# Kernel tuning notes

Hardware: AMD Instinct MI355X
Metric: run time of the kernel (lower is better)

The kernel has to match this reference:

```python
import jax, jax.numpy as jnp
import numpy as np


def _gelu(v):
    return jax.nn.gelu(v, approximate=False)


def _conv1x1(x, W, b):
    # x: [B, Ci, H, W], W: [Co, Ci]
    return jnp.einsum('bixy,oi->boxy', x, W) + b[None, :, None, None]


def _spectral(x, w1r, w2r, m1, m2):
    # x: [B, Ci, H, W]; w*r: [Ci, Co, m1, m2, 2] (real/imag)
    w1 = w1r[..., 0] + 1j * w1r[..., 1]
    w2 = w2r[..., 0] + 1j * w2r[..., 1]
    B, C, H, W = x.shape
    xf = jnp.fft.rfft2(x)  # [B, Ci, H, W//2+1] complex64
    o1 = jnp.einsum('bixy,ioxy->boxy', xf[:, :, :m1, :m2], w1)
    o2 = jnp.einsum('bixy,ioxy->boxy', xf[:, :, H - m1:, :m2], w2)
    Co = w1.shape[1]
    of = jnp.zeros((B, Co, H, W // 2 + 1), dtype=xf.dtype)
    of = of.at[:, :, :m1, :m2].set(o1)
    of = of.at[:, :, H - m1:, :m2].set(o2)
    return jnp.fft.irfft2(of, s=(H, W))


def _pool(x):
    B, C, H, W = x.shape
    return x.reshape(B, C, H // 2, 2, W // 2, 2).mean(axis=(3, 5))


def _up(x):
    # matches torch F.interpolate(scale_factor=2, mode='bilinear', align_corners=False)
    B, C, H, W = x.shape
    return jax.image.resize(x, (B, C, 2 * H, 2 * W), method='bilinear')


def _forward(x, fcin_w, fcin_b, sc1_w1, sc1_w2, c1_w, c1_b, sc2_w1, sc2_w2, c2_w, c2_b,
             scb_w1, scb_w2, cb_w, cb_b, su2_w1, su2_w2, u2_w, u2_b,
             su1_w1, su1_w2, u1_w, u1_b, fc1_w, fc1_b, fc2_w, fc2_b):
    v = jnp.einsum('bhwi,oi->bhwo', x, fcin_w) + fcin_b   # lift 6 -> width
    v = v.transpose(0, 3, 1, 2)                            # [B, C, H, W]
    x1 = _gelu(_spectral(v, sc1_w1, sc1_w2, 12, 12) + _conv1x1(v, c1_w, c1_b))
    x1d = _pool(x1)
    x2 = _gelu(_spectral(x1d, sc2_w1, sc2_w2, 8, 8) + _conv1x1(x1d, c2_w, c2_b))
    x2d = _pool(x2)
    xb = _gelu(_spectral(x2d, scb_w1, scb_w2, 4, 4) + _conv1x1(x2d, cb_w, cb_b))
    x2c = jnp.concatenate([_up(xb), x2], axis=1)           # [B, 3.5w, H/2, W/2]
    x2o = _gelu(_spectral(x2c, su2_w1, su2_w2, 8, 8) + _conv1x1(x2c, u2_w, u2_b))
    x1c = jnp.concatenate([_up(x2o), x1], axis=1)          # [B, 2.5w, H, W]
    x1o = _gelu(_spectral(x1c, su1_w1, su1_w2, 12, 12) + _conv1x1(x1c, u1_w, u1_b))
    h = x1o.transpose(0, 2, 3, 1)
    h = _gelu(jnp.einsum('bhwi,oi->bhwo', h, fc1_w) + fc1_b)
    return jnp.einsum('bhwi,oi->bhwo', h, fc2_w) + fc2_b   # [B, H, W, 3]


def setup_inputs() -> dict:
    key = jax.random.key(0)
    ks = jax.random.split(key, 20)

    def cw(k, ci, co, m):  # complex spectral weight stored as [...,2] real
        return (1.0 / (ci * co)) * jax.random.normal(k, (ci, co, m, m, 2), dtype=jnp.float32)

    def lin(k, o, i):
        k1, k2 = jax.random.split(k)
        lim = 1.0 / np.sqrt(i)
        return (jax.random.uniform(k1, (o, i), jnp.float32, -lim, lim),
                jax.random.uniform(k2, (o,), jnp.float32, -lim, lim))

    d = {}
    d['x'] = jax.random.normal(ks[0], (4, 256, 256, 6), dtype=jnp.float32)
    d['fcin_w'], d['fcin_b'] = lin(ks[1], 64, 6)
    d['sc1_w1'] = cw(ks[2], 64, 64, 12); d['sc1_w2'] = cw(ks[3], 64, 64, 12)
    d['c1_w'], d['c1_b'] = lin(ks[4], 64, 64)
    d['sc2_w1'] = cw(ks[5], 64, 96, 8); d['sc2_w2'] = cw(ks[6], 64, 96, 8)
    d['c2_w'], d['c2_b'] = lin(ks[7], 96, 64)
    d['scb_w1'] = cw(ks[8], 96, 128, 4); d['scb_w2'] = cw(ks[9], 96, 128, 4)
    d['cb_w'], d['cb_b'] = lin(ks[10], 128, 96)
    d['su2_w1'] = cw(ks[11], 224, 96, 8); d['su2_w2'] = cw(ks[12], 224, 96, 8)
    d['u2_w'], d['u2_b'] = lin(ks[13], 96, 224)
    d['su1_w1'] = cw(ks[14], 160, 64, 12); d['su1_w2'] = cw(ks[15], 160, 64, 12)
    d['u1_w'], d['u1_b'] = lin(ks[16], 64, 160)
    d['fc1_w'], d['fc1_b'] = lin(ks[17], 256, 64)
    d['fc2_w'], d['fc2_b'] = lin(ks[18], 3, 256)
    return d


def reference(x, fcin_w, fcin_b, sc1_w1, sc1_w2, c1_w, c1_b, sc2_w1, sc2_w2, c2_w, c2_b,
              scb_w1, scb_w2, cb_w, cb_b, su2_w1, su2_w2, u2_w, u2_b,
              su1_w1, su1_w2, u1_w, u1_b, fc1_w, fc1_b, fc2_w, fc2_b):
    return _forward(x, fcin_w, fcin_b, sc1_w1, sc1_w2, c1_w, c1_b, sc2_w1, sc2_w2, c2_w, c2_b,
                    scb_w1, scb_w2, cb_w, cb_b, su2_w1, su2_w2, u2_w, u2_b,
                    su1_w1, su1_w2, u1_w, u1_b, fc1_w, fc1_b, fc2_w, fc2_b)
```

## Files before the change

### kernel.cpp

```cpp
#include <hip/hip_runtime.h>
#include <math.h>
#include <cstdio>


__device__ __forceinline__ float gelu_f(float v) {
    return 0.5f * v * (1.0f + erff(v * 0.70710678118654752f));
}

__global__ __launch_bounds__(256) void init_tw_kernel(float2* tw) {
    int t = threadIdx.x;
    tw[t] = make_float2(cospif(t * (1.0f / 128.0f)), sinpif(t * (1.0f / 128.0f)));
}

__global__ __launch_bounds__(256) void transpose_mat_kernel(const float* __restrict__ src,
                                                            float* __restrict__ dst,
                                                            int Co, int Ci) {
    int idx = blockIdx.x * blockDim.x + threadIdx.x;
    if (idx >= Ci * Co) return;
    int o = idx % Co; int i = idx / Co;
    dst[idx] = src[(size_t)o * Ci + i];
}

template <int M2, int SRC>
__global__ __launch_bounds__(64, 4) void dftx_kernel(
    const float* __restrict__ U, int C, int Coff, int Ctot,
    int H, int W, int Hs, int Ws,
    const float* __restrict__ liftW, const float* __restrict__ liftB,
    int stepW, const float2* __restrict__ tw, float2* __restrict__ Fx) {
    __shared__ float twc[256], tws[256];
    for (int t = threadIdx.x; t < 256; t += blockDim.x) {
        float2 v = tw[t]; twc[t] = v.x; tws[t] = v.y;
    }
    __syncthreads();
    int by = blockIdx.x;
    int c = blockIdx.y * 64 + threadIdx.x;
    if (c >= C) return;

    const float* rowD = nullptr;
    const float* Sa = nullptr; const float* Sb = nullptr;
    float wy = 0.f, bc = 0.f;
    float w6[6] = {0, 0, 0, 0, 0, 0};
    if constexpr (SRC == 0) {
        rowD = U + (size_t)by * W * C + c;
    } else if constexpr (SRC == 1) {
        bc = liftB[c];
#pragma unroll
        for (int j = 0; j < 6; j++) w6[j] = liftW[c * 6 + j];
    } else {
        int b = by / H, y = by % H;
        float fy = 0.5f * y - 0.25f;
        int y0 = (int)floorf(fy); wy = fy - y0;
        int ya = y0 < 0 ? 0 : y0;
        int yb = (y0 + 1 > Hs - 1) ? Hs - 1 : y0 + 1;
        Sa = U + ((size_t)(b * Hs + ya) * Ws) * C + c;
        Sb = U + ((size_t)(b * Hs + yb) * Ws) * C + c;
    }

    float ar[M2], ai[M2];
#pragma unroll
    for (int k = 0; k < M2; k++) { ar[k] = 0.f; ai[k] = 0.f; }
    for (int x = 0; x < W; x++) {
        float u;
        if constexpr (SRC == 0) {
            u = rowD[(size_t)x * C];
        } else if constexpr (SRC == 1) {
            const float* xp = U + ((size_t)by * W + x) * 6;
            u = bc;
#pragma unroll
            for (int j = 0; j < 6; j++) u += w6[j] * xp[j];
        } else {
            float fx = 0.5f * x - 0.25f;
            int x0 = (int)floorf(fx); float wx = fx - x0;
            int xa = x0 < 0 ? 0 : x0;
            int xb2 = (x0 + 1 > Ws - 1) ? Ws - 1 : x0 + 1;
            float va = Sa[(size_t)xa * C] * (1.f - wx) + Sa[(size_t)xb2 * C] * wx;
            float vb = Sb[(size_t)xa * C] * (1.f - wx) + Sb[(size_t)xb2 * C] * wx;
            u = va * (1.f - wy) + vb * wy;
        }
        int tb = (x * stepW) & 255;
        int t = 0;
#pragma unroll
        for (int k = 0; k < M2; k++) {
            ar[k] += u * twc[t];
            ai[k] -= u * tws[t];
            t = (t + tb) & 255;
        }
    }
    float2* o = Fx + ((size_t)by * M2) * Ctot + Coff + c;
#pragma unroll
    for (int k = 0; k < M2; k++) o[(size_t)k * Ctot] = make_float2(ar[k], ai[k]);
}

__global__ __launch_bounds__(256, 4) void dfty_kernel(
    const float2* __restrict__ Fx, int H, int m1, int m2, int Ct,
    int stepH, const float2* __restrict__ tw, float2* __restrict__ XF, int N) {
    __shared__ float twc[256], tws[256];
    for (int t = threadIdx.x; t < 256; t += blockDim.x) {
        float2 v = tw[t]; twc[t] = v.x; tws[t] = v.y;
    }
    __syncthreads();
    int idx = blockIdx.x * blockDim.x + threadIdx.x;
    if (idx >= N) return;
    int c = idx % Ct; int r = idx / Ct;
    int kx = r % m2;  r /= m2;
    int kyi = r % (2 * m1); int b = r / (2 * m1);
    int ky = (kyi < m1) ? kyi : (H - 2 * m1 + kyi);
    int tstep = (ky * stepH) & 255;
    const float2* base = Fx + ((size_t)(b * H) * m2 + kx) * Ct + c;
    size_t stride = (size_t)m2 * Ct;
    float accr = 0.f, acci = 0.f;
    int t = 0;
    for (int y = 0; y < H; y++) {
        float2 f = base[(size_t)y * stride];
        float cc = twc[t], ss = tws[t];
        accr += f.x * cc + f.y * ss;
        acci += f.y * cc - f.x * ss;
        t = (t + tstep) & 255;
    }
    XF[idx] = make_float2(accr, acci);
}

__global__ __launch_bounds__(128, 2) void modemix2_kernel(
    const float2* __restrict__ XF,
    const float* __restrict__ w1f, const float* __restrict__ w2f,
    int Ci, int Co, int m1, int m2, float2* __restrict__ OF) {
    __shared__ float2 xsm[4][224];
    int mode = blockIdx.x;
    int nmode = 2 * m1 * m2;
    for (int t = threadIdx.x; t < 4 * Ci; t += blockDim.x) {
        int b = t / Ci, i = t - b * Ci;
        xsm[b][i] = XF[((size_t)b * nmode + mode) * Ci + i];
    }
    __syncthreads();
    int o = threadIdx.x;
    if (o >= Co) return;
    int kx = mode % m2; int kyi = mode / m2;
    const float2* w = (const float2*)((kyi < m1) ? w1f : w2f);
    int ky = (kyi < m1) ? kyi : (kyi - m1);
    float ar0 = 0, ai0 = 0, ar1 = 0, ai1 = 0, ar2 = 0, ai2 = 0, ar3 = 0, ai3 = 0;
    for (int i = 0; i < Ci; i++) {
        float2 wv = w[(((size_t)i * Co + o) * m1 + ky) * m2 + kx];
        float2 a = xsm[0][i], b2 = xsm[1][i], c2 = xsm[2][i], d2 = xsm[3][i];
        ar0 += a.x * wv.x - a.y * wv.y;  ai0 += a.x * wv.y + a.y * wv.x;
        ar1 += b2.x * wv.x - b2.y * wv.y; ai1 += b2.x * wv.y + b2.y * wv.x;
        ar2 += c2.x * wv.x - c2.y * wv.y; ai2 += c2.x * wv.y + c2.y * wv.x;
        ar3 += d2.x * wv.x - d2.y * wv.y; ai3 += d2.x * wv.y + d2.y * wv.x;
    }
    OF[((size_t)0 * nmode + mode) * Co + o] = make_float2(ar0, ai0);
    OF[((size_t)1 * nmode + mode) * Co + o] = make_float2(ar1, ai1);
    OF[((size_t)2 * nmode + mode) * Co + o] = make_float2(ar2, ai2);
    OF[((size_t)3 * nmode + mode) * Co + o] = make_float2(ar3, ai3);
}

__global__ __launch_bounds__(256, 4) void idfty_kernel(
    const float2* __restrict__ OF, int H, int m1, int m2, int Co,
    int stepH, const float2* __restrict__ tw, float2* __restrict__ Gy, int N) {
    __shared__ float twc[256], tws[256];
    for (int t = threadIdx.x; t < 256; t += blockDim.x) {
        float2 v = tw[t]; twc[t] = v.x; tws[t] = v.y;
    }
    __syncthreads();
    int idx = blockIdx.x * blockDim.x + threadIdx.x;
    if (idx >= N) return;
    int o = idx % Co; int r = idx / Co;
    int kx = r % m2;  r /= m2;
    int y = r % H;    int b = r / H;
    float accr = 0.f, acci = 0.f;
    for (int kyi = 0; kyi < 2 * m1; kyi++) {
        int ky = (kyi < m1) ? kyi : (H - 2 * m1 + kyi);
        int t = (ky * y * stepH) & 255;
        float2 f = OF[((size_t)(b * 2 * m1 + kyi) * m2 + kx) * Co + o];
        float cc = twc[t], ss = tws[t];
        accr += f.x * cc - f.y * ss;
        acci += f.x * ss + f.y * cc;
    }
    Gy[idx] = make_float2(accr, acci);
}

template <int SRCA, bool HASB, bool HEAD, int CO, int G, int PPG, int CIMAX>
__global__ __launch_bounds__(CO * G, 2) void synth_kernel(
    const float2* __restrict__ Gy,
    const float* __restrict__ A, int CA, int HsA, int WsA,
    const float* __restrict__ UB, int CB,
    const float* __restrict__ liftW, const float* __restrict__ liftB,
    const float* __restrict__ WcT, const float* __restrict__ bias,
    int H, int W, int m2, int stepW, float invHW,
    const float2* __restrict__ tw, float* __restrict__ out,
    const float* __restrict__ fc1t, const float* __restrict__ fc1b,
    const float* __restrict__ fc2w, const float* __restrict__ fc2b) {
    constexpr int P = G * PPG;
    constexpr int BLK = CO * G;
    __shared__ float twc[256], tws[256];
    __shared__ float xs[P][CIMAX];
    __shared__ float hid[HEAD ? P * 256 : 1];
    int tid = threadIdx.x;
    for (int t = tid; t < 256; t += BLK) {
        float2 v = tw[t]; twc[t] = v.x; tws[t] = v.y;
    }
    const int Ci = CA + (HASB ? CB : 0);
    int pix0 = blockIdx.x * P;
    for (int t = tid; t < P * Ci; t += BLK) {
        int p = t / Ci, i = t - p * Ci;
        int pix = pix0 + p;
        float val;
        if (HASB && i >= CA) {
            val = UB[(size_t)pix * CB + (i - CA)];
        } else if constexpr (SRCA == 0) {
            val = A[(size_t)pix * CA + i];
        } else if constexpr (SRCA == 1) {
            const float* xp = A + (size_t)pix * 6;
            float a = liftB[i];
#pragma unroll
            for (int j = 0; j < 6; j++) a += xp[j] * liftW[i * 6 + j];
            val = a;
        } else {
            int x = pix % W; int r = pix / W; int y = r % H; int b = r / H;
            float fy = 0.5f * y - 0.25f, fx = 0.5f * x - 0.25f;
            int y0 = (int)floorf(fy); float wy = fy - y0;
            int x0 = (int)floorf(fx); float wx = fx - x0;
            int ya = y0 < 0 ? 0 : y0;
            int yb = (y0 + 1 > HsA - 1) ? HsA - 1 : y0 + 1;
            int xa = x0 < 0 ? 0 : x0;
            int xb2 = (x0 + 1 > WsA - 1) ? WsA - 1 : x0 + 1;
            const float* base = A + ((size_t)b * HsA * WsA) * CA + i;
            float v00 = base[((size_t)ya * WsA + xa) * CA];
            float v01 = base[((size_t)ya * WsA + xb2) * CA];
            float v10 = base[((size_t)yb * WsA + xa) * CA];
            float v11 = base[((size_t)yb * WsA + xb2) * CA];
            val = (1.f - wy) * ((1.f - wx) * v00 + wx * v01) +
                  wy * ((1.f - wx) * v10 + wx * v11);
        }
        xs[p][i] = val;
    }
    __syncthreads();
    int o = tid % CO, g = tid / CO;
    int x0 = pix0 % W;  int by = pix0 / W;
    int xg = x0 + g * PPG;
    float acc[PPG];
#pragma unroll
    for (int q = 0; q < PPG; q++) acc[q] = 0.f;
    const float2* grow = Gy + ((size_t)by * m2) * CO + o;
    int base = (xg * stepW) & 255;
    for (int k = 0; k < m2; k++) {
        float2 gv = grow[(size_t)k * CO];
        float sc = (k == 0) ? 1.f : 2.f;
        float gx = sc * gv.x, gyv = sc * gv.y;
        int dk = (k * stepW) & 255;
        int t = (base * k) & 255;
#pragma unroll
        for (int q = 0; q < PPG; q++) {
            acc[q] += gx * twc[t] - gyv * tws[t];
            t = (t + dk) & 255;
        }
    }
#pragma unroll
    for (int q = 0; q < PPG; q++) acc[q] *= invHW;
    for (int i = 0; i < Ci; i++) {
        float w = WcT[(size_t)i * CO + o];
#pragma unroll
        for (int q = 0; q < PPG; q++) acc[q] += xs[g * PPG + q][i] * w;
    }
    float bb = bias[o];
    if constexpr (!HEAD) {
#pragma unroll
        for (int q = 0; q < PPG; q++) {
            int pix = pix0 + g * PPG + q;
            out[(size_t)pix * CO + o] = gelu_f(acc[q] + bb);
        }
    } else {
        float gout[PPG];
#pragma unroll
        for (int q = 0; q < PPG; q++) gout[q] = gelu_f(acc[q] + bb);
        __syncthreads();
        float* act = &xs[0][0];
#pragma unroll
        for (int q = 0; q < PPG; q++) act[(g * PPG + q) * 64 + o] = gout[q];
        __syncthreads();
        int j = tid;
        float h[P];
        float c1 = fc1b[j];
#pragma unroll
        for (int p = 0; p < P; p++) h[p] = c1;
        for (int i = 0; i < 64; i++) {
            float w = fc1t[i * 256 + j];
#pragma unroll
            for (int p = 0; p < P; p++) h[p] += act[p * 64 + i] * w;
        }
#pragma unroll
        for (int p = 0; p < P; p++) hid[p * 256 + j] = gelu_f(h[p]);
        __syncthreads();
        if (tid < P * 12) {
            int sub = tid & 3; int d = tid >> 2;
            int o3 = d % 3, p = d / 3;
            const float* hr = hid + p * 256;
            const float* wr = fc2w + o3 * 256;
            float a = 0.f;
            for (int i = sub; i < 256; i += 4) a += hr[i] * wr[i];
            a += __shfl_xor(a, 1);
            a += __shfl_xor(a, 2);
            if (sub == 0) out[(size_t)(pix0 + p) * 3 + o3] = a + fc2b[o3];
        }
    }
}

__global__ __launch_bounds__(256, 4) void pool_kernel(
    const float* __restrict__ in, float* __restrict__ out,
    int H2, int W2, int C, int N) {
    int idx = blockIdx.x * blockDim.x + threadIdx.x;
    if (idx >= N) return;
    int c = idx % C; int r = idx / C;
    int xo = r % W2; r /= W2;
    int yo = r % H2; int b = r / H2;
    int W = W2 * 2;
    const float* p = in + (((size_t)(b * (H2 * 2) + 2 * yo) * W) + 2 * xo) * C + c;
    float v = p[0] + p[C] + p[(size_t)W * C] + p[(size_t)W * C + C];
    out[idx] = 0.25f * v;
}


static inline unsigned nb_(size_t n, int b) { return (unsigned)((n + b - 1) / b); }

extern "C" void kernel_launch(void* const* d_in, const int* in_sizes, int n_in,
                              void* d_out, int out_size, void* d_ws, size_t ws_size,
                              hipStream_t stream) {
    (void)in_sizes; (void)n_in; (void)out_size;
    const float* x      = (const float*)d_in[0];
    const float* fcin_w = (const float*)d_in[1];
    const float* fcin_b = (const float*)d_in[2];
    const float* sc1_w1 = (const float*)d_in[3];
    const float* sc1_w2 = (const float*)d_in[4];
    const float* c1_w   = (const float*)d_in[5];
    const float* c1_b   = (const float*)d_in[6];
    const float* sc2_w1 = (const float*)d_in[7];
    const float* sc2_w2 = (const float*)d_in[8];
    const float* c2_w   = (const float*)d_in[9];
    const float* c2_b   = (const float*)d_in[10];
    const float* scb_w1 = (const float*)d_in[11];
    const float* scb_w2 = (const float*)d_in[12];
    const float* cb_w   = (const float*)d_in[13];
    const float* cb_b   = (const float*)d_in[14];
    const float* su2_w1 = (const float*)d_in[15];
    const float* su2_w2 = (const float*)d_in[16];
    const float* u2_w   = (const float*)d_in[17];
    const float* u2_b   = (const float*)d_in[18];
    const float* su1_w1 = (const float*)d_in[19];
    const float* su1_w2 = (const float*)d_in[20];
    const float* u1_w   = (const float*)d_in[21];
    const float* u1_b   = (const float*)d_in[22];
    const float* fc1_w  = (const float*)d_in[23];
    const float* fc1_b  = (const float*)d_in[24];
    const float* fc2_w  = (const float*)d_in[25];
    const float* fc2_b  = (const float*)d_in[26];
    float* out = (float*)d_out;

    float* wsf = (float*)d_ws;
    size_t off = 0;
    auto alloc = [&](size_t nfloats) -> float* {
        float* p = wsf + off;
        off += (nfloats + 63) & ~(size_t)63;
        return p;
    };

    float2* tw = (float2*)alloc(512);
    float* c1t  = alloc(64 * 64);
    float* c2t  = alloc(64 * 96);
    float* cbt  = alloc(96 * 128);
    float* u2t  = alloc(224 * 96);
    float* u1t  = alloc(160 * 64);
    float* fc1t = alloc(64 * 256);

    float* x1  = alloc((size_t)4 * 256 * 256 * 64);
    float* x1d = alloc((size_t)4 * 128 * 128 * 64);
    float* x2  = alloc((size_t)4 * 128 * 128 * 96);
    float* xb  = alloc((size_t)4 * 64 * 64 * 128);
    float* x2o = alloc((size_t)4 * 128 * 128 * 96);

    float2* Fx = (float2*)alloc((size_t)2 * 4 * 256 * 12 * 160);
    float2* XF = (float2*)alloc((size_t)2 * 4 * 24 * 12 * 160);
    float2* OF = (float2*)alloc((size_t)2 * 4 * 24 * 12 * 128);
    float2* Gy = (float2*)alloc((size_t)2 * 4 * 256 * 12 * 96);

    size_t need = off * sizeof(float);
    if (ws_size < need) {
        fprintf(stderr, "[FNO2d] workspace too small: need %zu bytes, have %zu\n",
                need, ws_size);
        return;
    }
    float* x2d = x1d;

    init_tw_kernel<<<1, 256, 0, stream>>>(tw);
    transpose_mat_kernel<<<nb_(64 * 64, 256), 256, 0, stream>>>(c1_w, c1t, 64, 64);
    transpose_mat_kernel<<<nb_(64 * 96, 256), 256, 0, stream>>>(c2_w, c2t, 96, 64);
    transpose_mat_kernel<<<nb_(96 * 128, 256), 256, 0, stream>>>(cb_w, cbt, 128, 96);
    transpose_mat_kernel<<<nb_(224 * 96, 256), 256, 0, stream>>>(u2_w, u2t, 96, 224);
    transpose_mat_kernel<<<nb_(160 * 64, 256), 256, 0, stream>>>(u1_w, u1t, 64, 160);
    transpose_mat_kernel<<<nb_(64 * 256, 256), 256, 0, stream>>>(fc1_w, fc1t, 256, 64);

    int N;

    dftx_kernel<12, 1><<<dim3(1024, 1), 64, 0, stream>>>(
        x, 64, 0, 64, 256, 256, 0, 0, fcin_w, fcin_b, 1, tw, Fx);
    N = 4 * 24 * 12 * 64;
    dfty_kernel<<<nb_(N, 256), 256, 0, stream>>>(Fx, 256, 12, 12, 64, 1, tw, XF, N);
    modemix2_kernel<<<288, 128, 0, stream>>>(XF, sc1_w1, sc1_w2, 64, 64, 12, 12, OF);
    N = 4 * 256 * 12 * 64;
    idfty_kernel<<<nb_(N, 256), 256, 0, stream>>>(OF, 256, 12, 12, 64, 1, tw, Gy, N);
    synth_kernel<1, false, false, 64, 4, 4, 64><<<4 * 256 * 256 / 16, 256, 0, stream>>>(
        Gy, x, 64, 0, 0, nullptr, 0, fcin_w, fcin_b, c1t, c1_b,
        256, 256, 12, 1, 1.0f / 65536.0f, tw, x1,
        nullptr, nullptr, nullptr, nullptr);
    N = 4 * 128 * 128 * 64;
    pool_kernel<<<nb_(N, 256), 256, 0, stream>>>(x1, x1d, 128, 128, 64, N);

    dftx_kernel<8, 0><<<dim3(512, 1), 64, 0, stream>>>(
        x1d, 64, 0, 64, 128, 128, 0, 0, nullptr, nullptr, 2, tw, Fx);
    N = 4 * 16 * 8 * 64;
    dfty_kernel<<<nb_(N, 256), 256, 0, stream>>>(Fx, 128, 8, 8, 64, 2, tw, XF, N);
    modemix2_kernel<<<128, 128, 0, stream>>>(XF, sc2_w1, sc2_w2, 64, 96, 8, 8, OF);
    N = 4 * 128 * 8 * 96;
    idfty_kernel<<<nb_(N, 256), 256, 0, stream>>>(OF, 128, 8, 8, 96, 2, tw, Gy, N);
    synth_kernel<0, false, false, 96, 2, 4, 64><<<4 * 128 * 128 / 8, 192, 0, stream>>>(
        Gy, x1d, 64, 0, 0, nullptr, 0, nullptr, nullptr, c2t, c2_b,
        128, 128, 8, 2, 1.0f / 16384.0f, tw, x2,
        nullptr, nullptr, nullptr, nullptr);
    N = 4 * 64 * 64 * 96;
    pool_kernel<<<nb_(N, 256), 256, 0, stream>>>(x2, x2d, 64, 64, 96, N);

    dftx_kernel<4, 0><<<dim3(256, 2), 64, 0, stream>>>(
        x2d, 96, 0, 96, 64, 64, 0, 0, nullptr, nullptr, 4, tw, Fx);
    N = 4 * 8 * 4 * 96;
    dfty_kernel<<<nb_(N, 256), 256, 0, stream>>>(Fx, 64, 4, 4, 96, 4, tw, XF, N);
    modemix2_kernel<<<32, 128, 0, stream>>>(XF, scb_w1, scb_w2, 96, 128, 4, 4, OF);
    N = 4 * 64 * 4 * 128;
    idfty_kernel<<<nb_(N, 256), 256, 0, stream>>>(OF, 64, 4, 4, 128, 4, tw, Gy, N);
    synth_kernel<0, false, false, 128, 2, 4, 96><<<4 * 64 * 64 / 8, 256, 0, stream>>>(
        Gy, x2d, 96, 0, 0, nullptr, 0, nullptr, nullptr, cbt, cb_b,
        64, 64, 4, 4, 1.0f / 4096.0f, tw, xb,
        nullptr, nullptr, nullptr, nullptr);

    dftx_kernel<8, 2><<<dim3(512, 2), 64, 0, stream>>>(
        xb, 128, 0, 224, 128, 128, 64, 64, nullptr, nullptr, 2, tw, Fx);
    dftx_kernel<8, 0><<<dim3(512, 2), 64, 0, stream>>>(
        x2, 96, 128, 224, 128, 128, 0, 0, nullptr, nullptr, 2, tw, Fx);
    N = 4 * 16 * 8 * 224;
    dfty_kernel<<<nb_(N, 256), 256, 0, stream>>>(Fx, 128, 8, 8, 224, 2, tw, XF, N);
    modemix2_kernel<<<128, 128, 0, stream>>>(XF, su2_w1, su2_w2, 224, 96, 8, 8, OF);
    N = 4 * 128 * 8 * 96;
    idfty_kernel<<<nb_(N, 256), 256, 0, stream>>>(OF, 128, 8, 8, 96, 2, tw, Gy, N);
    synth_kernel<2, true, false, 96, 2, 4, 224><<<4 * 128 * 128 / 8, 192, 0, stream>>>(
        Gy, xb, 128, 64, 64, x2, 96, nullptr, nullptr, u2t, u2_b,
        128, 128, 8, 2, 1.0f / 16384.0f, tw, x2o,
        nullptr, nullptr, nullptr, nullptr);

    dftx_kernel<12, 2><<<dim3(1024, 2), 64, 0, stream>>>(
        x2o, 96, 0, 160, 256, 256, 128, 128, nullptr, nullptr, 1, tw, Fx);
    dftx_kernel<12, 0><<<dim3(1024, 1), 64, 0, stream>>>(
        x1, 64, 96, 160, 256, 256, 0, 0, nullptr, nullptr, 1, tw, Fx);
    N = 4 * 24 * 12 * 160;
    dfty_kernel<<<nb_(N, 256), 256, 0, stream>>>(Fx, 256, 12, 12, 160, 1, tw, XF, N);
    modemix2_kernel<<<288, 128, 0, stream>>>(XF, su1_w1, su1_w2, 160, 64, 12, 12, OF);
    N = 4 * 256 * 12 * 64;
    idfty_kernel<<<nb_(N, 256), 256, 0, stream>>>(OF, 256, 12, 12, 64, 1, tw, Gy, N);
    synth_kernel<2, true, true, 64, 4, 4, 160><<<4 * 256 * 256 / 16, 256, 0, stream>>>(
        Gy, x2o, 96, 128, 128, x1, 64, nullptr, nullptr, u1t, u1_b,
        256, 256, 12, 1, 1.0f / 65536.0f, tw, out,
        fc1t, fc1_b, fc2_w, fc2_b);
}
```

Before: 1.773 ms.

## Precompute per-block twiddle tables and vectorize channel-mix dot products

```diff
diff --git a/kernel.cpp b/kernel.cpp
--- a/kernel.cpp
+++ b/kernel.cpp
@@ -7,33 +7,31 @@
     return 0.5f * v * (1.0f + erff(v * 0.70710678118654752f));
 }
 
+__device__ __forceinline__ float dot4(float4 a, float4 b) {
+    return a.x * b.x + a.y * b.y + a.z * b.z + a.w * b.w;
+}
+
 __global__ __launch_bounds__(256) void init_tw_kernel(float2* tw) {
     int t = threadIdx.x;
     tw[t] = make_float2(cospif(t * (1.0f / 128.0f)), sinpif(t * (1.0f / 128.0f)));
 }
 
-__global__ __launch_bounds__(256) void transpose_mat_kernel(const float* __restrict__ src,
-                                                            float* __restrict__ dst,
-                                                            int Co, int Ci) {
-    int idx = blockIdx.x * blockDim.x + threadIdx.x;
-    if (idx >= Ci * Co) return;
-    int o = idx % Co; int i = idx / Co;
-    dst[idx] = src[(size_t)o * Ci + i];
-}
-
-template <int M2, int SRC>
-__global__ __launch_bounds__(64, 4) void dftx_kernel(
+template <int M2, int SRC, int W_T>
+__global__ __launch_bounds__(256, 4) void dftx_kernel(
     const float* __restrict__ U, int C, int Coff, int Ctot,
-    int H, int W, int Hs, int Ws,
+    int H, int Hs, int Ws,
     const float* __restrict__ liftW, const float* __restrict__ liftB,
     int stepW, const float2* __restrict__ tw, float2* __restrict__ Fx) {
-    __shared__ float twc[256], tws[256];
-    for (int t = threadIdx.x; t < 256; t += blockDim.x) {
-        float2 v = tw[t]; twc[t] = v.x; tws[t] = v.y;
+    constexpr int W = W_T;
+    __shared__ float2 twxk[W * M2];
+    int tid = threadIdx.x;
+    for (int t = tid; t < W * M2; t += 256) {
+        int x = t / M2, k = t - (t / M2) * M2;
+        twxk[t] = tw[(x * k * stepW) & 255];
     }
     __syncthreads();
-    int by = blockIdx.x;
-    int c = blockIdx.y * 64 + threadIdx.x;
+    int by = blockIdx.x * 4 + (tid >> 6);
+    int c = blockIdx.y * 64 + (tid & 63);
     if (c >= C) return;
 
     const float* rowD = nullptr;
@@ -77,13 +75,12 @@
             float vb = Sb[(size_t)xa * C] * (1.f - wx) + Sb[(size_t)xb2 * C] * wx;
             u = va * (1.f - wy) + vb * wy;
         }
-        int tb = (x * stepW) & 255;
-        int t = 0;
-#pragma unroll
-        for (int k = 0; k < M2; k++) {
-            ar[k] += u * twc[t];
-            ai[k] -= u * tws[t];
-            t = (t + tb) & 255;
+        const float4* wp = (const float4*)&twxk[x * M2];
+#pragma unroll
+        for (int k2 = 0; k2 < M2 / 2; k2++) {
+            float4 t4 = wp[k2];
+            ar[2 * k2] += u * t4.x;     ai[2 * k2] -= u * t4.y;
+            ar[2 * k2 + 1] += u * t4.z; ai[2 * k2 + 1] -= u * t4.w;
         }
     }
     float2* o = Fx + ((size_t)by * M2) * Ctot + Coff + c;
@@ -177,28 +174,30 @@
     Gy[idx] = make_float2(accr, acci);
 }
 
-template <int SRCA, bool HASB, bool HEAD, int CO, int G, int PPG, int CIMAX>
+template <int SRCA, bool HASB, bool HEAD, int CO, int G, int PPG, int CIMAX, int M2>
 __global__ __launch_bounds__(CO * G, 2) void synth_kernel(
     const float2* __restrict__ Gy,
     const float* __restrict__ A, int CA, int HsA, int WsA,
     const float* __restrict__ UB, int CB,
     const float* __restrict__ liftW, const float* __restrict__ liftB,
-    const float* __restrict__ WcT, const float* __restrict__ bias,
-    int H, int W, int m2, int stepW, float invHW,
+    const float* __restrict__ Wc, const float* __restrict__ bias,
+    int H, int W, int stepW, float invHW,
     const float2* __restrict__ tw, float* __restrict__ out,
-    const float* __restrict__ fc1t, const float* __restrict__ fc1b,
+    const float* __restrict__ fc1w, const float* __restrict__ fc1b,
     const float* __restrict__ fc2w, const float* __restrict__ fc2b) {
     constexpr int P = G * PPG;
     constexpr int BLK = CO * G;
-    __shared__ float twc[256], tws[256];
     __shared__ float xs[P][CIMAX];
+    __shared__ float2 twp[P][M2];
     __shared__ float hid[HEAD ? P * 256 : 1];
     int tid = threadIdx.x;
-    for (int t = tid; t < 256; t += BLK) {
-        float2 v = tw[t]; twc[t] = v.x; tws[t] = v.y;
+    int pix0 = blockIdx.x * P;
+    int x0 = pix0 % W;  int by = pix0 / W;
+    for (int t = tid; t < P * M2; t += BLK) {
+        int p = t / M2, k = t - (t / M2) * M2;
+        twp[p][k] = tw[((x0 + p) * k * stepW) & 255];
     }
     const int Ci = CA + (HASB ? CB : 0);
-    int pix0 = blockIdx.x * P;
     for (int t = tid; t < P * Ci; t += BLK) {
         int p = t / Ci, i = t - p * Ci;
         int pix = pix0 + p;
@@ -217,11 +216,11 @@
             int x = pix % W; int r = pix / W; int y = r % H; int b = r / H;
             float fy = 0.5f * y - 0.25f, fx = 0.5f * x - 0.25f;
             int y0 = (int)floorf(fy); float wy = fy - y0;
-            int x0 = (int)floorf(fx); float wx = fx - x0;
+            int x0i = (int)floorf(fx); float wx = fx - x0i;
             int ya = y0 < 0 ? 0 : y0;
             int yb = (y0 + 1 > HsA - 1) ? HsA - 1 : y0 + 1;
-            int xa = x0 < 0 ? 0 : x0;
-            int xb2 = (x0 + 1 > WsA - 1) ? WsA - 1 : x0 + 1;
+            int xa = x0i < 0 ? 0 : x0i;
+            int xb2 = (x0i + 1 > WsA - 1) ? WsA - 1 : x0i + 1;
             const float* base = A + ((size_t)b * HsA * WsA) * CA + i;
             float v00 = base[((size_t)ya * WsA + xa) * CA];
             float v01 = base[((size_t)ya * WsA + xb2) * CA];
@@ -234,31 +233,30 @@
     }
     __syncthreads();
     int o = tid % CO, g = tid / CO;
-    int x0 = pix0 % W;  int by = pix0 / W;
-    int xg = x0 + g * PPG;
     float acc[PPG];
 #pragma unroll
     for (int q = 0; q < PPG; q++) acc[q] = 0.f;
-    const float2* grow = Gy + ((size_t)by * m2) * CO + o;
-    int base = (xg * stepW) & 255;
-    for (int k = 0; k < m2; k++) {
+    const float2* grow = Gy + ((size_t)by * M2) * CO + o;
+    for (int k = 0; k < M2; k++) {
         float2 gv = grow[(size_t)k * CO];
         float sc = (k == 0) ? 1.f : 2.f;
         float gx = sc * gv.x, gyv = sc * gv.y;
-        int dk = (k * stepW) & 255;
-        int t = (base * k) & 255;
 #pragma unroll
         for (int q = 0; q < PPG; q++) {
-            acc[q] += gx * twc[t] - gyv * tws[t];
-            t = (t + dk) & 255;
+            float2 wq = twp[g * PPG + q][k];
+            acc[q] += gx * wq.x - gyv * wq.y;
         }
     }
 #pragma unroll
     for (int q = 0; q < PPG; q++) acc[q] *= invHW;
-    for (int i = 0; i < Ci; i++) {
-        float w = WcT[(size_t)i * CO + o];
-#pragma unroll
-        for (int q = 0; q < PPG; q++) acc[q] += xs[g * PPG + q][i] * w;
+    const float4* wrow = (const float4*)(Wc + (size_t)o * Ci);
+    for (int i4 = 0; i4 < Ci / 4; i4++) {
+        float4 wv = wrow[i4];
+#pragma unroll
+        for (int q = 0; q < PPG; q++) {
+            float4 a = *(const float4*)&xs[g * PPG + q][i4 * 4];
+            acc[q] += dot4(a, wv);
+        }
     }
     float bb = bias[o];
     if constexpr (!HEAD) {
@@ -281,10 +279,15 @@
         float c1 = fc1b[j];
 #pragma unroll
         for (int p = 0; p < P; p++) h[p] = c1;
-        for (int i = 0; i < 64; i++) {
-            float w = fc1t[i * 256 + j];
-#pragma unroll
-            for (int p = 0; p < P; p++) h[p] += act[p * 64 + i] * w;
+        const float4* wj = (const float4*)(fc1w + (size_t)j * 64);
+#pragma unroll 2
+        for (int i4 = 0; i4 < 16; i4++) {
+            float4 wv = wj[i4];
+#pragma unroll
+            for (int p = 0; p < P; p++) {
+                float4 a = *(const float4*)&act[p * 64 + i4 * 4];
+                h[p] += dot4(a, wv);
+            }
         }
 #pragma unroll
         for (int p = 0; p < P; p++) hid[p * 256 + j] = gelu_f(h[p]);
@@ -362,12 +365,6 @@
     };
 
     float2* tw = (float2*)alloc(512);
-    float* c1t  = alloc(64 * 64);
-    float* c2t  = alloc(64 * 96);
-    float* cbt  = alloc(96 * 128);
-    float* u2t  = alloc(224 * 96);
-    float* u1t  = alloc(160 * 64);
-    float* fc1t = alloc(64 * 256);
 
     float* x1  = alloc((size_t)4 * 256 * 256 * 64);
     float* x1d = alloc((size_t)4 * 128 * 128 * 64);
@@ -389,80 +386,74 @@
     float* x2d = x1d;
 
     init_tw_kernel<<<1, 256, 0, stream>>>(tw);
-    transpose_mat_kernel<<<nb_(64 * 64, 256), 256, 0, stream>>>(c1_w, c1t, 64, 64);
-    transpose_mat_kernel<<<nb_(64 * 96, 256), 256, 0, stream>>>(c2_w, c2t, 96, 64);
-    transpose_mat_kernel<<<nb_(96 * 128, 256), 256, 0, stream>>>(cb_w, cbt, 128, 96);
-    transpose_mat_kernel<<<nb_(224 * 96, 256), 256, 0, stream>>>(u2_w, u2t, 96, 224);
-    transpose_mat_kernel<<<nb_(160 * 64, 256), 256, 0, stream>>>(u1_w, u1t, 64, 160);
-    transpose_mat_kernel<<<nb_(64 * 256, 256), 256, 0, stream>>>(fc1_w, fc1t, 256, 64);
 
     int N;
 
-    dftx_kernel<12, 1><<<dim3(1024, 1), 64, 0, stream>>>(
-        x, 64, 0, 64, 256, 256, 0, 0, fcin_w, fcin_b, 1, tw, Fx);
+    dftx_kernel<12, 1, 256><<<dim3(256, 1), 256, 0, stream>>>(
+        x, 64, 0, 64, 256, 0, 0, fcin_w, fcin_b, 1, tw, Fx);
     N = 4 * 24 * 12 * 64;
     dfty_kernel<<<nb_(N, 256), 256, 0, stream>>>(Fx, 256, 12, 12, 64, 1, tw, XF, N);
     modemix2_kernel<<<288, 128, 0, stream>>>(XF, sc1_w1, sc1_w2, 64, 64, 12, 12, OF);
     N = 4 * 256 * 12 * 64;
     idfty_kernel<<<nb_(N, 256), 256, 0, stream>>>(OF, 256, 12, 12, 64, 1, tw, Gy, N);
-    synth_kernel<1, false, false, 64, 4, 4, 64><<<4 * 256 * 256 / 16, 256, 0, stream>>>(
-        Gy, x, 64, 0, 0, nullptr, 0, fcin_w, fcin_b, c1t, c1_b,
-        256, 256, 12, 1, 1.0f / 65536.0f, tw, x1,
+    synth_kernel<1, false, false, 64, 4, 4, 64, 12><<<4 * 256 * 256 / 16, 256, 0, stream>>>(
+        Gy, x, 64, 0, 0, nullptr, 0, fcin_w, fcin_b, c1_w, c1_b,
+        256, 256, 1, 1.0f / 65536.0f, tw, x1,
         nullptr, nullptr, nullptr, nullptr);
     N = 4 * 128 * 128 * 64;
     pool_kernel<<<nb_(N, 256), 256, 0, stream>>>(x1, x1d, 128, 128, 64, N);
 
-    dftx_kernel<8, 0><<<dim3(512, 1), 64, 0, stream>>>(
-        x1d, 64, 0, 64, 128, 128, 0, 0, nullptr, nullptr, 2, tw, Fx);
+    dftx_kernel<8, 0, 128><<<dim3(128, 1), 256, 0, stream>>>(
+        x1d, 64, 0, 64, 128, 0, 0, nullptr, nullptr, 2, tw, Fx);
     N = 4 * 16 * 8 * 64;
     dfty_kernel<<<nb_(N, 256), 256, 0, stream>>>(Fx, 128, 8, 8, 64, 2, tw, XF, N);
     modemix2_kernel<<<128, 128, 0, stream>>>(XF, sc2_w1, sc2_w2, 64, 96, 8, 8, OF);
     N = 4 * 128 * 8 * 96;
     idfty_kernel<<<nb_(N, 256), 256, 0, stream>>>(OF, 128, 8, 8, 96, 2, tw, Gy, N);
-    synth_kernel<0, false, false, 96, 2, 4, 64><<<4 * 128 * 128 / 8, 192, 0, stream>>>(
-        Gy, x1d, 64, 0, 0, nullptr, 0, nullptr, nullptr, c2t, c2_b,
-        128, 128, 8, 2, 1.0f / 16384.0f, tw, x2,
+    synth_kernel<0, false, false, 96, 2, 4, 64, 8><<<4 * 128 * 128 / 8, 192, 0, stream>>>(
+        Gy, x1d, 64, 0, 0, nullptr, 0, nullptr, nullptr, c2_w, c2_b,
+        128, 128, 2, 1.0f / 16384.0f, tw, x2,
         nullptr, nullptr, nullptr, nullptr);
     N = 4 * 64 * 64 * 96;
     pool_kernel<<<nb_(N, 256), 256, 0, stream>>>(x2, x2d, 64, 64, 96, N);
 
-    dftx_kernel<4, 0><<<dim3(256, 2), 64, 0, stream>>>(
-        x2d, 96, 0, 96, 64, 64, 0, 0, nullptr, nullptr, 4, tw, Fx);
+    dftx_kernel<4, 0, 64><<<dim3(64, 2), 256, 0, stream>>>(
+        x2d, 96, 0, 96, 64, 0, 0, nullptr, nullptr, 4, tw, Fx);
     N = 4 * 8 * 4 * 96;
     dfty_kernel<<<nb_(N, 256), 256, 0, stream>>>(Fx, 64, 4, 4, 96, 4, tw, XF, N);
     modemix2_kernel<<<32, 128, 0, stream>>>(XF, scb_w1, scb_w2, 96, 128, 4, 4, OF);
     N = 4 * 64 * 4 * 128;
     idfty_kernel<<<nb_(N, 256), 256, 0, stream>>>(OF, 64, 4, 4, 128, 4, tw, Gy, N);
-    synth_kernel<0, false, false, 128, 2, 4, 96><<<4 * 64 * 64 / 8, 256, 0, stream>>>(
-        Gy, x2d, 96, 0, 0, nullptr, 0, nullptr, nullptr, cbt, cb_b,
-        64, 64, 4, 4, 1.0f / 4096.0f, tw, xb,
+    synth_kernel<0, false, false, 128, 2, 4, 96, 4><<<4 * 64 * 64 / 8, 256, 0, stream>>>(
+        Gy, x2d, 96, 0, 0, nullptr, 0, nullptr, nullptr, cb_w, cb_b,
+        64, 64, 4, 1.0f / 4096.0f, tw, xb,
         nullptr, nullptr, nullptr, nullptr);
 
-    dftx_kernel<8, 2><<<dim3(512, 2), 64, 0, stream>>>(
-        xb, 128, 0, 224, 128, 128, 64, 64, nullptr, nullptr, 2, tw, Fx);
-    dftx_kernel<8, 0><<<dim3(512, 2), 64, 0, stream>>>(
-        x2, 96, 128, 224, 128, 128, 0, 0, nullptr, nullptr, 2, tw, Fx);
+    dftx_kernel<8, 2, 128><<<dim3(128, 2), 256, 0, stream>>>(
+        xb, 128, 0, 224, 128, 64, 64, nullptr, nullptr, 2, tw, Fx);
+    dftx_kernel<8, 0, 128><<<dim3(128, 2), 256, 0, stream>>>(
+        x2, 96, 128, 224, 128, 0, 0, nullptr, nullptr, 2, tw, Fx);
     N = 4 * 16 * 8 * 224;
     dfty_kernel<<<nb_(N, 256), 256, 0, stream>>>(Fx, 128, 8, 8, 224, 2, tw, XF, N);
     modemix2_kernel<<<128, 128, 0, stream>>>(XF, su2_w1, su2_w2, 224, 96, 8, 8, OF);
     N = 4 * 128 * 8 * 96;
     idfty_kernel<<<nb_(N, 256), 256, 0, stream>>>(OF, 128, 8, 8, 96, 2, tw, Gy, N);
-    synth_kernel<2, true, false, 96, 2, 4, 224><<<4 * 128 * 128 / 8, 192, 0, stream>>>(
-        Gy, xb, 128, 64, 64, x2, 96, nullptr, nullptr, u2t, u2_b,
-        128, 128, 8, 2, 1.0f / 16384.0f, tw, x2o,
+    synth_kernel<2, true, false, 96, 2, 4, 224, 8><<<4 * 128 * 128 / 8, 192, 0, stream>>>(
+        Gy, xb, 128, 64, 64, x2, 96, nullptr, nullptr, u2_w, u2_b,
+        128, 128, 2, 1.0f / 16384.0f, tw, x2o,
         nullptr, nullptr, nullptr, nullptr);
 
-    dftx_kernel<12, 2><<<dim3(1024, 2), 64, 0, stream>>>(
-        x2o, 96, 0, 160, 256, 256, 128, 128, nullptr, nullptr, 1, tw, Fx);
-    dftx_kernel<12, 0><<<dim3(1024, 1), 64, 0, stream>>>(
-        x1, 64, 96, 160, 256, 256, 0, 0, nullptr, nullptr, 1, tw, Fx);
+    dftx_kernel<12, 2, 256><<<dim3(256, 2), 256, 0, stream>>>(
+        x2o, 96, 0, 160, 256, 128, 128, nullptr, nullptr, 1, tw, Fx);
+    dftx_kernel<12, 0, 256><<<dim3(256, 1), 256, 0, stream>>>(
+        x1, 64, 96, 160, 256, 0, 0, nullptr, nullptr, 1, tw, Fx);
     N = 4 * 24 * 12 * 160;
     dfty_kernel<<<nb_(N, 256), 256, 0, stream>>>(Fx, 256, 12, 12, 160, 1, tw, XF, N);
     modemix2_kernel<<<288, 128, 0, stream>>>(XF, su1_w1, su1_w2, 160, 64, 12, 12, OF);
     N = 4 * 256 * 12 * 64;
     idfty_kernel<<<nb_(N, 256), 256, 0, stream>>>(OF, 256, 12, 12, 64, 1, tw, Gy, N);
-    synth_kernel<2, true, true, 64, 4, 4, 160><<<4 * 256 * 256 / 16, 256, 0, stream>>>(
-        Gy, x2o, 96, 128, 128, x1, 64, nullptr, nullptr, u1t, u1_b,
-        256, 256, 12, 1, 1.0f / 65536.0f, tw, out,
-        fc1t, fc1_b, fc2_w, fc2_b);
-}
+    synth_kernel<2, true, true, 64, 4, 4, 160, 12><<<4 * 256 * 256 / 16, 256, 0, stream>>>(
+        Gy, x2o, 96, 128, 128, x1, 64, nullptr, nullptr, u1_w, u1_b,
+        256, 256, 1, 1.0f / 65536.0f, tw, out,
+        fc1_w, fc1_b, fc2_w, fc2_b);
+}
```

Result: slower. 2.114 ms (+19.2%).
